# Kernel tuning notes

Hardware: AMD Instinct MI355X
Metric: run time of the kernel (lower is better)

Reference implementation:

```python
import jax, jax.numpy as jnp
import numpy as np

N_TAPERS = 3  # standard edgetaper iteration count used in vdeblur

def psf2otf(psf, shape):
    # zero-pad psf to `shape` and circularly shift so kernel center -> (0,0), then FFT
    kh, kw = psf.shape[-2], psf.shape[-1]
    pad = [(0, 0)] * (psf.ndim - 2) + [(0, shape[0] - kh), (0, shape[1] - kw)]
    p = jnp.pad(psf, pad)
    p = jnp.roll(p, shift=(-(kh // 2), -(kw // 2)), axis=(-2, -1))
    return jnp.fft.fft2(p)

def edgetaper_alpha(kernel, shape):
    # kernel: [kh,kw]; builds the separable taper window from kernel autocorrelation
    vs = []
    for i in range(2):
        proj = jnp.sum(kernel, axis=1 - i)
        z = jnp.fft.fft(proj, shape[i] - 1)
        z = jnp.fft.ifft(jnp.abs(z) ** 2).real
        z = jnp.concatenate([z, z[:1]])
        vs.append(1.0 - z / jnp.max(z))
    return jnp.outer(vs[0], vs[1])

def edgetaper_one(img, kernel):
    # img: [C,Hp,Wp], kernel: [kh,kw]; blend image with its circular blur near borders
    shape = img.shape[-2:]
    alpha = edgetaper_alpha(kernel, shape)[None]          # [1,Hp,Wp]
    otf = psf2otf(kernel, shape)[None]                    # [1,Hp,Wp] complex
    for _ in range(N_TAPERS):
        blurred = jnp.fft.ifft2(jnp.fft.fft2(img) * otf).real
        img = alpha * img + (1.0 - alpha) * blurred
    return img

def setup_inputs() -> dict:
    key = jax.random.key(0)
    k1, k2, k3, k4 = jax.random.split(key, 4)
    B, C, H, W = 8, 3, 512, 512
    KH = KW = 31
    NF, FS = 8, 3
    y = jax.random.uniform(k1, (B, C, H, W), dtype=jnp.float32)
    k = jax.random.uniform(k2, (B, 1, KH, KW), dtype=jnp.float32)
    k = k / jnp.sum(k, axis=(-2, -1), keepdims=True)       # normalized blur PSF
    lam = jax.random.uniform(k3, (), dtype=jnp.float32)    # nn.Parameter(torch.rand(1).squeeze())
    fan_in = C * FS * FS
    filters = jax.random.normal(k4, (NF, C, FS, FS), dtype=jnp.float32) * np.sqrt(2.0 / fan_in)
    return {"y": y, "k": k, "lam": lam, "filters": filters}

def reference(y, k, lam, filters):
    kh, kw = k.shape[-2], k.shape[-1]
    ph, pw = (kh - 1) // 2, (kw - 1) // 2
    # pad_for_kernel (edge replicate) + edgetaper
    x = jnp.pad(y, ((0, 0), (0, 0), (ph, ph), (pw, pw)), mode='edge')
    x = jax.vmap(edgetaper_one)(x, k[:, 0])
    H, W = x.shape[-2], x.shape[-1]
    Fy = jnp.fft.fft2(x)                                   # [B,C,H,W] complex (== rfft onesided=False)
    Dg = psf2otf(filters, (H, W))                          # [NF,C,H,W]
    Dk = psf2otf(k, (H, W))                                # [B,1,H,W], broadcasts over C
    exp_lam = jnp.exp(lam)
    Dg_sum = jnp.sum(jnp.abs(Dg) ** 2, axis=0)[None] * exp_lam   # [1,C,H,W]
    Omega = 1.0 / (jnp.abs(Dk) ** 2 + Dg_sum)              # [B,C,H,W]
    out = jnp.fft.ifft2(Omega * jnp.conj(Dk) * Fy).real    # irfft onesided=False
    return out
```

## Files before the change

### kernel.cpp

```cpp
#include <hip/hip_runtime.h>
#include <cmath>

#define HH 542
#define KH 271
#define NPIX (HH*HH)
#define RS 544
#define PPIX (HH*RS)
#define BB 8
#define CC3 3
#define NCH (BB*CC3)
#define NP 12
#define MROWS (NP*HH)
#define KSZ 31
#define KRAD 15
#define NF 8
#define FS 3

#define NSPLIT 2
#define NGRP 40
#define BTSZ (NGRP*NSPLIT*17*512)

typedef __attribute__((ext_vector_type(8))) short short8v;
typedef __attribute__((ext_vector_type(4))) float float4v;

static __device__ __forceinline__ float2 cmul(float2 a, float2 b) {
    return make_float2(a.x*b.x - a.y*b.y, a.x*b.y + a.y*b.x);
}

static __device__ __forceinline__ void pair_chans(int p, int& n1, int& n2) {
    if (p < 8) { n1 = 3*p;     n2 = 3*p + 1; }
    else       { int q = p-8; n1 = 6*q + 2; n2 = 6*q + 5; }
}

static __device__ __forceinline__ void split2_pack_pair(float x, float y,
        unsigned& p0, unsigned& p1) {
    unsigned ux = __float_as_uint(x), uy = __float_as_uint(y);
    unsigned hx0 = (ux + 0x8000u) & 0xffff0000u;
    unsigned hy0 = (uy + 0x8000u) & 0xffff0000u;
    float rx = x - __uint_as_float(hx0);
    float ry = y - __uint_as_float(hy0);
    unsigned hx1 = (__float_as_uint(rx) + 0x8000u) & 0xffff0000u;
    unsigned hy1 = (__float_as_uint(ry) + 0x8000u) & 0xffff0000u;
    p0 = (hx0 >> 16) | hy0;
    p1 = (hx1 >> 16) | hy1;
}

__global__ void gen_tables(float2* tw542, short* Btf, short* Bti) {
    int idx = blockIdx.x*blockDim.x + threadIdx.x;
    const float PI2 = 6.283185307179586f;
    if (idx < HH) {
        float ang = -PI2*(float)idx/(float)HH;
        float s, c; sincosf(ang, &s, &c);
        tw542[idx] = make_float2(c, s);
    }
    if (idx >= BTSZ) return;
    int j    = idx & 7;
    int lane = (idx >> 3) & 63;
    int rem  = idx >> 9;
    int step = rem % 17;
    int rem2 = rem / 17;
    int s    = rem2 % NSPLIT;
    int g    = rem2 / NSPLIT;
    if (g >= NGRP) return;
    int o  = (g >= 20) ? 1 : 0;
    int v1 = (g - 20*o)*16 + (lane & 15);
    int kq = step*32 + (lane >> 4)*8 + j;
    int kidx = kq >> 1, c = kq & 1;
    float wre = 0.f, wim = 0.f;
    if (v1 < KH && kidx < KH) {
        int r = (kidx*v1) % KH;
        float ang = -PI2*(float)r/(float)KH;
        float sn, cs; sincosf(ang, &sn, &cs);
        wre = cs; wim = sn;
    }
    float vf = (o==0) ? ((c==0) ? wre : -wim) : ((c==0) ?  wim : wre);
    float vi = (o==0) ? ((c==0) ? wre :  wim) : ((c==0) ? -wim : wre);
    {
        unsigned u = __float_as_uint(vf);
        unsigned h0 = (u + 0x8000u) & 0xffff0000u;
        float r1 = vf - __uint_as_float(h0);
        unsigned h1 = (__float_as_uint(r1) + 0x8000u) & 0xffff0000u;
        Btf[idx] = (short)(((s==0) ? h0 : h1) >> 16);
    }
    {
        unsigned u = __float_as_uint(vi);
        unsigned h0 = (u + 0x8000u) & 0xffff0000u;
        float r1 = vi - __uint_as_float(h0);
        unsigned h1 = (__float_as_uint(r1) + 0x8000u) & 0xffff0000u;
        Bti[idx] = (short)(((s==0) ? h0 : h1) >> 16);
    }
}

__global__ void alpha_kernel(const float* __restrict__ kk, float* __restrict__ valpha) {
    int b = blockIdx.x;
    int t = threadIdx.x;
    __shared__ float proj[2][KSZ];
    __shared__ float ac[2][KSZ];
    const float* kb = kk + b*KSZ*KSZ;
    if (t < KSZ) {
        float s = 0;
        for (int j = 0; j < KSZ; j++) s += kb[t*KSZ + j];
        proj[0][t] = s;
    } else if (t >= 32 && t < 32+KSZ) {
        int j = t - 32;
        float s = 0;
        for (int i = 0; i < KSZ; i++) s += kb[i*KSZ + j];
        proj[1][j] = s;
    }
    __syncthreads();
    if (t < KSZ) {
        float s0 = 0, s1 = 0;
        for (int m = 0; m + t < KSZ; m++) {
            s0 += proj[0][m]*proj[0][m+t];
            s1 += proj[1][m]*proj[1][m+t];
        }
        ac[0][t] = s0; ac[1][t] = s1;
    }
    __syncthreads();
    float inv0 = 1.0f/ac[0][0];
    float inv1 = 1.0f/ac[1][0];
    for (int d = t; d < HH; d += blockDim.x) {
        for (int a = 0; a < 2; a++) {
            float z;
            if (d <= 30)                   z = ac[a][d];
            else if (d >= 511 && d <= 540) z = ac[a][541-d];
            else if (d == 541)             z = ac[a][0];
            else                           z = 0.0f;
            valpha[(b*2 + a)*HH + d] = 1.0f - z*(a ? inv1 : inv0);
        }
    }
}

__global__ void dk_stage1(const float* __restrict__ kk, const float2* __restrict__ tw,
                          float2* __restrict__ T1) {
    int idx = blockIdx.x*blockDim.x + threadIdx.x;
    if (idx >= BB*KSZ*HH) return;
    int v  = idx % HH;
    int bm = idx / HH;
    int m  = bm % KSZ;
    int b  = bm / KSZ;
    const float* kb = kk + (b*KSZ + m)*KSZ;
    float2 w  = tw[(KRAD*(HH - v)) % HH];
    float2 ru = tw[v];
    float2 acc = make_float2(0.f, 0.f);
    for (int n = 0; n < KSZ; n++) {
        float kv = kb[n];
        acc.x = fmaf(kv, w.x, acc.x);
        acc.y = fmaf(kv, w.y, acc.y);
        float wx = w.x*ru.x - w.y*ru.y;
        float wy = w.x*ru.y + w.y*ru.x;
        w = make_float2(wx, wy);
    }
    T1[idx] = acc;
}

#define UT2 8
__global__ void dk_stage2(const float2* __restrict__ T1, const float2* __restrict__ tw,
                          float2* __restrict__ Dk) {
    int bid = blockIdx.x;
    int vc = bid % 3;
    int rem = bid / 3;
    int ut = rem % 68;
    int b  = rem / 68;
    int v = vc*256 + threadIdx.x;
    if (v >= HH) return;
    int u0 = ut*UT2;
    float2 acc[UT2], w[UT2], ru[UT2];
    #pragma unroll
    for (int uu = 0; uu < UT2; uu++) {
        int u = u0 + uu;
        int uc = (u < HH) ? u : 0;
        acc[uu] = make_float2(0.f, 0.f);
        w[uu]  = tw[(KRAD*(HH - uc)) % HH];
        ru[uu] = tw[uc];
    }
    const float2* t1 = T1 + (size_t)b*KSZ*HH + v;
    for (int m = 0; m < KSZ; m++) {
        float2 t = t1[(size_t)m*HH];
        #pragma unroll
        for (int uu = 0; uu < UT2; uu++) {
            acc[uu].x = fmaf(t.x, w[uu].x, fmaf(-t.y, w[uu].y, acc[uu].x));
            acc[uu].y = fmaf(t.x, w[uu].y, fmaf( t.y, w[uu].x, acc[uu].y));
            float wx = w[uu].x*ru[uu].x - w[uu].y*ru[uu].y;
            float wy = w[uu].x*ru[uu].y + w[uu].y*ru[uu].x;
            w[uu] = make_float2(wx, wy);
        }
    }
    #pragma unroll
    for (int uu = 0; uu < UT2; uu++) {
        int u = u0 + uu;
        if (u < HH) Dk[(size_t)b*NPIX + (size_t)u*HH + v] = acc[uu];
    }
}

__global__ void dgs_kernel(const float* __restrict__ filt, const float* __restrict__ lamp,
                           const float2* __restrict__ tw, float* __restrict__ Dgs) {
    int uv = blockIdx.x*blockDim.x + threadIdx.x;
    if (uv >= NPIX) return;
    int u = uv / HH;
    int v = uv - u*HH;
    float el = expf(lamp[0]);
    float2 wu[3], wv[3];
    wu[0] = tw[u ? HH-u : 0]; wu[1] = make_float2(1.f,0.f); wu[2] = tw[u];
    wv[0] = tw[v ? HH-v : 0]; wv[1] = make_float2(1.f,0.f); wv[2] = tw[v];
    float2 ph[3][3];
    #pragma unroll
    for (int m = 0; m < 3; m++)
        #pragma unroll
        for (int n = 0; n < 3; n++)
            ph[m][n] = cmul(wu[m], wv[n]);
    for (int c = 0; c < CC3; c++) {
        float s = 0.f;
        for (int f = 0; f < NF; f++) {
            float2 acc = make_float2(0.f, 0.f);
            const float* fp = filt + ((f*CC3 + c)*FS)*FS;
            #pragma unroll
            for (int m = 0; m < 3; m++)
                #pragma unroll
                for (int n = 0; n < 3; n++) {
                    float fv = fp[m*3+n];
                    acc.x = fmaf(fv, ph[m][n].x, acc.x);
                    acc.y = fmaf(fv, ph[m][n].y, acc.y);
                }
            s = fmaf(acc.x, acc.x, fmaf(acc.y, acc.y, s));
        }
        Dgs[c*NPIX + uv] = s*el;
    }
}

__global__ void pad_pack(const float* __restrict__ y, float* __restrict__ R0,
                         float2* __restrict__ CA) {
    int idx = blockIdx.x*blockDim.x + threadIdx.x;
    if (idx >= NP*NPIX) return;
    int uv = idx % NPIX;
    int p  = idx / NPIX;
    int n1, n2; pair_chans(p, n1, n2);
    int i = uv / HH, j = uv - i*HH;
    int yi = min(max(i - KRAD, 0), 511);
    int yj = min(max(j - KRAD, 0), 511);
    int yo = yi*512 + yj;
    float v1 = y[(size_t)n1*262144 + yo];
    float v2 = y[(size_t)n2*262144 + yo];
    size_t sp = (size_t)i*RS + j;
    R0[(size_t)n1*PPIX + sp] = v1;
    R0[(size_t)n2*PPIX + sp] = v2;
    CA[(size_t)p*PPIX + sp] = make_float2(v1, v2);
}

__global__ void specmul(const float2* __restrict__ CA, const float2* __restrict__ Dk,
                        const float* __restrict__ Dgs, float2* __restrict__ CB, int mode) {
    int idx = blockIdx.x*blockDim.x + threadIdx.x;
    if (idx >= NP*NPIX) return;
    int uv = idx % NPIX;
    int p  = idx / NPIX;
    int n1, n2; pair_chans(p, n1, n2);
    int b1 = n1/3, c1 = n1 - 3*b1;
    int b2 = n2/3, c2 = n2 - 3*b2;
    int i = uv / HH, j = uv - i*HH;
    int ni = i ? HH - i : 0;
    int nj = j ? HH - j : 0;
    float2 Z  = CA[(size_t)p*PPIX + (size_t)i*RS + j];
    float2 Zm = CA[(size_t)p*PPIX + (size_t)ni*RS + nj];
    float2 F1 = make_float2(0.5f*(Z.x + Zm.x), 0.5f*(Z.y - Zm.y));
    float2 F2 = make_float2(0.5f*(Z.y + Zm.y), 0.5f*(Zm.x - Z.x));
    float2 d1 = Dk[(size_t)b1*NPIX + uv];
    float2 d2 = Dk[(size_t)b2*NPIX + uv];
    float2 M1, M2;
    if (mode == 0) {
        M1 = d1; M2 = d2;
    } else {
        float o1 = 1.0f/(d1.x*d1.x + d1.y*d1.y + Dgs[(size_t)c1*NPIX + uv]);
        float o2 = 1.0f/(d2.x*d2.x + d2.y*d2.y + Dgs[(size_t)c2*NPIX + uv]);
        M1 = make_float2(d1.x*o1, -d1.y*o1);
        M2 = make_float2(d2.x*o2, -d2.y*o2);
    }
    float2 W1 = cmul(M1, F1);
    float2 W2 = cmul(M2, F2);
    CB[(size_t)p*PPIX + (size_t)i*RS + j] = make_float2(W1.x - W2.y, W1.y + W2.x);
}

__global__ void __launch_bounds__(256, 4)
fft_mfma(const float2* __restrict__ Ain, float2* __restrict__ Aout,
         const short* __restrict__ Bt, const float2* __restrict__ tw542,
         const float* __restrict__ valp, float* __restrict__ R0,
         float* __restrict__ outbuf, float scale, int conjtw, int mode)
{
    __shared__ char smem[17408];
    short* As = (short*)smem;
    float4* Tsf = (float4*)smem;
    const int APL = 64*40;

    int id = blockIdx.x;
    int xcd = id & 7, jj = id >> 3;
    int lin = xcd*128 + jj;
    if (lin >= 1020) return;
    int by = lin / 5, bx = lin - 5*by;

    int tid = threadIdx.x;
    int arow = tid >> 3, ai4 = tid & 7;
    int wid = tid >> 6, lane = tid & 63;
    int l15 = lane & 15, quad = lane >> 4;

    int aoff0 = l15*40 + quad*8;

    const short* pB[2];
    #pragma unroll
    for (int ct = 0; ct < 2; ct++) {
        int grp = (ct ? 20 : 0) + bx*4 + wid;
        pB[ct] = Bt + (size_t)grp*(NSPLIT*17*512) + lane*8;
    }

    float4v acc[4][2];
    #pragma unroll
    for (int mt = 0; mt < 4; mt++)
        #pragma unroll
        for (int ct = 0; ct < 2; ct++)
            acc[mt][ct] = (float4v)(0.f);

    float4 regA[2][2];
    short8v bf[2][2][2];
    const float4 z4 = make_float4(0.f,0.f,0.f,0.f);

    int rowg = by*32 + arow;
    bool rvld = rowg < MROWS;
    const float4* rp = (const float4*)Ain + (size_t)(rvld ? rowg : 0)*(RS/2);

    auto loadA = [&](int buf, int step) {
        int i0 = step*16 + 2*ai4;
        regA[buf][0] = (rvld && i0     < 271) ? rp[i0]   : z4;
        regA[buf][1] = (rvld && i0 + 1 < 271) ? rp[i0+1] : z4;
    };
    auto loadB = [&](int buf, int step) {
        #pragma unroll
        for (int ct = 0; ct < 2; ct++)
            #pragma unroll
            for (int s = 0; s < NSPLIT; s++)
                bf[buf][ct][s] = *(const short8v*)(pB[ct] + ((s*17 + step) << 9));
    };

    loadA(0, 0); loadB(0, 0);

    #pragma unroll 2
    for (int step = 0; step < 17; step++) {
        int cur = step & 1, nxt = cur ^ 1;
        {
            int rl = 2*arow;
            int offE = rl*40 + 4*ai4;
            float4 f0 = regA[cur][0], f1 = regA[cur][1];
            unsigned e0a,e1a, e0b,e1b;
            split2_pack_pair(f0.x, f0.y, e0a, e1a);
            split2_pack_pair(f1.x, f1.y, e0b, e1b);
            *(uint2*)(As + 0*APL + offE) = make_uint2(e0a, e0b);
            *(uint2*)(As + 1*APL + offE) = make_uint2(e1a, e1b);
            unsigned o0a,o1a, o0b,o1b;
            split2_pack_pair(f0.z, f0.w, o0a, o1a);
            split2_pack_pair(f1.z, f1.w, o0b, o1b);
            int offO = offE + 40;
            *(uint2*)(As + 0*APL + offO) = make_uint2(o0a, o0b);
            *(uint2*)(As + 1*APL + offO) = make_uint2(o1a, o1b);
        }
        __syncthreads();

        if (step + 1 < 17) { loadA(nxt, step+1); loadB(nxt, step+1); }

        #pragma unroll
        for (int sa = 0; sa < 2; sa++) {
            short8v af[4];
            #pragma unroll
            for (int mt = 0; mt < 4; mt++)
                af[mt] = *(const short8v*)(As + sa*APL + aoff0 + mt*16*40);
            #pragma unroll
            for (int sb = 0; sb + sa < 2; sb++)
                #pragma unroll
                for (int mt = 0; mt < 4; mt++)
                    #pragma unroll
                    for (int ct = 0; ct < 2; ct++)
                        acc[mt][ct] = __builtin_amdgcn_mfma_f32_16x16x32_bf16(
                            af[mt], bf[cur][ct][sb], acc[mt][ct], 0, 0, 0);
        }
        __syncthreads();
    }

    float2 tg;
    {
        int v1g = (bx*4 + wid)*16 + l15;
        tg = tw542[(v1g < HH) ? v1g : 0];
        if (conjtw) tg.y = -tg.y;
    }

    int lane16 = tid & 15;
    int rrow = tid >> 4;
    int r0 = by*32 + 2*lane16;
    bool rok = r0 < MROWS;
    int plane = rok ? (r0 / HH) : 0;
    int colg = r0 - plane*HH;
    int n1, n2; pair_chans(plane, n1, n2);
    int b1 = n1/3, b2 = n2/3;

    #pragma unroll
    for (int half = 0; half < 2; half++) {
        __syncthreads();
        #pragma unroll
        for (int mt = 0; mt < 4; mt++) {
            float2 v[2];
            #pragma unroll
            for (int pr = 0; pr < 2; pr++) {
                float Ere = acc[mt][0][2*pr], Ore = acc[mt][0][2*pr+1];
                float Eim = acc[mt][1][2*pr], Oim = acc[mt][1][2*pr+1];
                float tOre = tg.x*Ore - tg.y*Oim;
                float tOim = tg.x*Oim + tg.y*Ore;
                v[pr] = (half == 0)
                    ? make_float2((Ere + tOre)*scale, (Eim + tOim)*scale)
                    : make_float2((Ere - tOre)*scale, (Eim - tOim)*scale);
            }
            int v1loc = wid*16 + l15;
            int uu = mt*4 + quad;
            Tsf[v1loc*17 + uu] = make_float4(v[0].x, v[0].y, v[1].x, v[1].y);
        }
        __syncthreads();
        #pragma unroll
        for (int it = 0; it < 4; it++) {
            int v1loc = rrow + it*16;
            int v1g2 = bx*64 + v1loc;
            if (v1g2 >= KH || !rok) continue;
            int v1 = v1g2 + (half ? KH : 0);
            float4 f = Tsf[v1loc*17 + lane16];
            size_t sp = (size_t)v1*RS + colg;
            if (mode == 0) {
                *(float4*)(Aout + (size_t)plane*PPIX + sp) = f;
            } else if (mode == 1) {
                float ar1 = valp[b1*2*HH + v1];
                float ar2 = valp[b2*2*HH + v1];
                float ac1a = valp[(b1*2+1)*HH + colg];
                float ac1b = valp[(b1*2+1)*HH + colg + 1];
                float ac2a = valp[(b2*2+1)*HH + colg];
                float ac2b = valp[(b2*2+1)*HH + colg + 1];
                float2* p1 = (float2*)(R0 + (size_t)n1*PPIX + sp);
                float2* p2 = (float2*)(R0 + (size_t)n2*PPIX + sp);
                float2 o1 = *p1, o2 = *p2;
                float nv1a = fmaf(ar1*ac1a, o1.x - f.x, f.x);
                float nv1b = fmaf(ar1*ac1b, o1.y - f.z, f.z);
                float nv2a = fmaf(ar2*ac2a, o2.x - f.y, f.y);
                float nv2b = fmaf(ar2*ac2b, o2.y - f.w, f.w);
                *p1 = make_float2(nv1a, nv1b);
                *p2 = make_float2(nv2a, nv2b);
                *(float4*)(Aout + (size_t)plane*PPIX + sp) =
                    make_float4(nv1a, nv2a, nv1b, nv2b);
            } else {
                size_t so = (size_t)v1*HH + colg;
                *(float2*)(outbuf + (size_t)n1*NPIX + so) = make_float2(f.x, f.z);
                *(float2*)(outbuf + (size_t)n2*NPIX + so) = make_float2(f.y, f.w);
            }
        }
    }
}

extern "C" void kernel_launch(void* const* d_in, const int* in_sizes, int n_in,
                              void* d_out, int out_size, void* d_ws, size_t ws_size,
                              hipStream_t stream) {
    const float* y    = (const float*)d_in[0];
    const float* k    = (const float*)d_in[1];
    const float* lam  = (const float*)d_in[2];
    const float* filt = (const float*)d_in[3];
    float* out = (float*)d_out;

    char* base = (char*)d_ws;
    size_t off = 0;
    auto alloc = [&](size_t bytes) {
        void* p = base + off;
        off = (off + bytes + 511) & ~(size_t)511;
        return p;
    };
    float2* CA   = (float2*)alloc(sizeof(float2)*(size_t)NP*PPIX);
    float2* CB   = (float2*)alloc(sizeof(float2)*(size_t)NP*PPIX);
    float*  R0   = (float*) alloc(sizeof(float)*(size_t)NCH*PPIX);
    float2* Dk   = (float2*)alloc(sizeof(float2)*(size_t)BB*NPIX);
    float2* T1   = (float2*)alloc(sizeof(float2)*(size_t)BB*KSZ*HH);
    float*  Dgs  = (float*) alloc(sizeof(float)*(size_t)CC3*NPIX);
    short*  Btf  = (short*) alloc(sizeof(short)*(size_t)BTSZ);
    short*  Bti  = (short*) alloc(sizeof(short)*(size_t)BTSZ);
    float2* tw   = (float2*)alloc(sizeof(float2)*(size_t)HH);
    float*  valp = (float*) alloc(sizeof(float)*(size_t)BB*2*HH);
    (void)ws_size; (void)in_sizes; (void)n_in; (void)out_size;

    const int TPB = 256;
    auto nb = [](long n) { return (int)((n + 255)/256); };

    gen_tables<<<nb((long)BTSZ), TPB, 0, stream>>>(tw, Btf, Bti);
    alpha_kernel<<<BB, 64, 0, stream>>>(k, valp);
    dk_stage1<<<nb((long)BB*KSZ*HH), TPB, 0, stream>>>(k, tw, T1);
    dk_stage2<<<8*68*3, TPB, 0, stream>>>(T1, tw, Dk);
    dgs_kernel<<<nb((long)NPIX), TPB, 0, stream>>>(filt, lam, tw, Dgs);
    pad_pack<<<nb((long)NP*NPIX), TPB, 0, stream>>>(y, R0, CA);

    const int FG = 1024;
    const float isc = 1.0f/(float)HH;
    float2 *S = CA, *T = CB;
    fft_mfma<<<FG, TPB, 0, stream>>>(S, T, Btf, tw, valp, R0, out, 1.0f, 0, 0);
    fft_mfma<<<FG, TPB, 0, stream>>>(T, S, Btf, tw, valp, R0, out, 1.0f, 0, 0);
    for (int it = 0; it < 3; it++) {
        specmul<<<nb((long)NP*NPIX), TPB, 0, stream>>>(S, Dk, Dgs, T, 0);
        fft_mfma<<<FG, TPB, 0, stream>>>(T, S, Bti, tw, valp, R0, out, isc, 1, 0);
        fft_mfma<<<FG, TPB, 0, stream>>>(S, T, Bti, tw, valp, R0, out, isc, 1, 1);
        fft_mfma<<<FG, TPB, 0, stream>>>(T, S, Btf, tw, valp, R0, out, 1.0f, 0, 0);
        fft_mfma<<<FG, TPB, 0, stream>>>(S, T, Btf, tw, valp, R0, out, 1.0f, 0, 0);
        float2* tmp = S; S = T; T = tmp;
    }
    specmul<<<nb((long)NP*NPIX), TPB, 0, stream>>>(S, Dk, Dgs, T, 1);
    fft_mfma<<<FG, TPB, 0, stream>>>(T, S, Bti, tw, valp, R0, out, isc, 1, 0);
    fft_mfma<<<FG, TPB, 0, stream>>>(S, T, Bti, tw, valp, R0, out, isc, 1, 2);
}
```

Before: 749.3 us.

## Store intermediate FFT planes pre-split into bf16 hi/lo in MFMA-ready layout

Intermediate complex planes are now stored as pre-split bf16 hi/lo pairs, arranged so that fft_mfma can load A fragments straight from global memory into MFMA registers. This removes the LDS staging, the per-step split/pack work and the two __syncthreads per K step inside the GEMM loop. Producers (pad_pack, specmul, the fft epilogue) now do the split when they write, and specmul reconstructs floats when it reads. The buffers are zeroed with memsets so the padded rows and columns read as zero. In exchange, the A-operand loads lose the old software prefetch double-buffering and the global reads become more scattered.

```diff
diff --git a/kernel.cpp b/kernel.cpp
--- a/kernel.cpp
+++ b/kernel.cpp
@@ -16,6 +16,10 @@
 #define NF 8
 #define FS 3
 
+#define SROW 544
+#define SROWS_PL 13056
+#define SPL ((size_t)SROWS_PL*SROW)
+
 #define NSPLIT 2
 #define NGRP 40
 #define BTSZ (NGRP*NSPLIT*17*512)
@@ -43,6 +47,12 @@
     unsigned hy1 = (__float_as_uint(ry) + 0x8000u) & 0xffff0000u;
     p0 = (hx0 >> 16) | hy0;
     p1 = (hx1 >> 16) | hy1;
+}
+
+static __device__ __forceinline__ float2 unsplit_pair(unsigned h, unsigned l) {
+    float x = __uint_as_float(h << 16) + __uint_as_float(l << 16);
+    float y = __uint_as_float(h & 0xffff0000u) + __uint_as_float(l & 0xffff0000u);
+    return make_float2(x, y);
 }
 
 __global__ void gen_tables(float2* tw542, short* Btf, short* Bti) {
@@ -229,7 +239,7 @@
 }
 
 __global__ void pad_pack(const float* __restrict__ y, float* __restrict__ R0,
-                         float2* __restrict__ CA) {
+                         short* __restrict__ CAs) {
     int idx = blockIdx.x*blockDim.x + threadIdx.x;
     if (idx >= NP*NPIX) return;
     int uv = idx % NPIX;
@@ -241,14 +251,17 @@
     int yo = yi*512 + yj;
     float v1 = y[(size_t)n1*262144 + yo];
     float v2 = y[(size_t)n2*262144 + yo];
-    size_t sp = (size_t)i*RS + j;
-    R0[(size_t)n1*PPIX + sp] = v1;
-    R0[(size_t)n2*PPIX + sp] = v2;
-    CA[(size_t)p*PPIX + sp] = make_float2(v1, v2);
-}
-
-__global__ void specmul(const float2* __restrict__ CA, const float2* __restrict__ Dk,
-                        const float* __restrict__ Dgs, float2* __restrict__ CB, int mode) {
+    R0[(size_t)n1*PPIX + (size_t)i*RS + j] = v1;
+    R0[(size_t)n2*PPIX + (size_t)i*RS + j] = v2;
+    unsigned hi, lo; split2_pack_pair(v1, v2, hi, lo);
+    size_t row = 2*((size_t)p*HH + i) + (size_t)(j & 1);
+    size_t col = (size_t)(j & ~1);
+    *(unsigned*)(CAs + row*SROW + col)       = hi;
+    *(unsigned*)(CAs + SPL + row*SROW + col) = lo;
+}
+
+__global__ void specmul(const short* __restrict__ CAs, const float2* __restrict__ Dk,
+                        const float* __restrict__ Dgs, short* __restrict__ CBs, int mode) {
     int idx = blockIdx.x*blockDim.x + threadIdx.x;
     if (idx >= NP*NPIX) return;
     int uv = idx % NPIX;
@@ -259,8 +272,16 @@
     int i = uv / HH, j = uv - i*HH;
     int ni = i ? HH - i : 0;
     int nj = j ? HH - j : 0;
-    float2 Z  = CA[(size_t)p*PPIX + (size_t)i*RS + j];
-    float2 Zm = CA[(size_t)p*PPIX + (size_t)ni*RS + nj];
+    size_t rz = 2*((size_t)p*HH + i) + (size_t)(j & 1);
+    size_t cz = (size_t)(j & ~1);
+    size_t rm = 2*((size_t)p*HH + ni) + (size_t)(nj & 1);
+    size_t cm = (size_t)(nj & ~1);
+    unsigned zh = *(const unsigned*)(CAs + rz*SROW + cz);
+    unsigned zl = *(const unsigned*)(CAs + SPL + rz*SROW + cz);
+    unsigned mh = *(const unsigned*)(CAs + rm*SROW + cm);
+    unsigned ml = *(const unsigned*)(CAs + SPL + rm*SROW + cm);
+    float2 Z  = unsplit_pair(zh, zl);
+    float2 Zm = unsplit_pair(mh, ml);
     float2 F1 = make_float2(0.5f*(Z.x + Zm.x), 0.5f*(Z.y - Zm.y));
     float2 F2 = make_float2(0.5f*(Z.y + Zm.y), 0.5f*(Zm.x - Z.x));
     float2 d1 = Dk[(size_t)b1*NPIX + uv];
@@ -276,19 +297,19 @@
     }
     float2 W1 = cmul(M1, F1);
     float2 W2 = cmul(M2, F2);
-    CB[(size_t)p*PPIX + (size_t)i*RS + j] = make_float2(W1.x - W2.y, W1.y + W2.x);
+    float2 out = make_float2(W1.x - W2.y, W1.y + W2.x);
+    unsigned hi, lo; split2_pack_pair(out.x, out.y, hi, lo);
+    *(unsigned*)(CBs + rz*SROW + cz)       = hi;
+    *(unsigned*)(CBs + SPL + rz*SROW + cz) = lo;
 }
 
 __global__ void __launch_bounds__(256, 4)
-fft_mfma(const float2* __restrict__ Ain, float2* __restrict__ Aout,
+fft_mfma(const short* __restrict__ Ains, short* __restrict__ Aouts,
          const short* __restrict__ Bt, const float2* __restrict__ tw542,
          const float* __restrict__ valp, float* __restrict__ R0,
          float* __restrict__ outbuf, float scale, int conjtw, int mode)
 {
-    __shared__ char smem[17408];
-    short* As = (short*)smem;
-    float4* Tsf = (float4*)smem;
-    const int APL = 64*40;
+    __shared__ float4 Tsf[64*17];
 
     int id = blockIdx.x;
     int xcd = id & 7, jj = id >> 3;
@@ -297,11 +318,17 @@
     int by = lin / 5, bx = lin - 5*by;
 
     int tid = threadIdx.x;
-    int arow = tid >> 3, ai4 = tid & 7;
     int wid = tid >> 6, lane = tid & 63;
     int l15 = lane & 15, quad = lane >> 4;
 
-    int aoff0 = l15*40 + quad*8;
+    const short* pA[2][4];
+    #pragma unroll
+    for (int sa = 0; sa < 2; sa++)
+        #pragma unroll
+        for (int mt = 0; mt < 4; mt++) {
+            size_t rl = (size_t)by*64 + (size_t)(l15 + mt*16);
+            pA[sa][mt] = Ains + (size_t)sa*SPL + rl*SROW + quad*8;
+        }
 
     const short* pB[2];
     #pragma unroll
@@ -317,58 +344,21 @@
         for (int ct = 0; ct < 2; ct++)
             acc[mt][ct] = (float4v)(0.f);
 
-    float4 regA[2][2];
-    short8v bf[2][2][2];
-    const float4 z4 = make_float4(0.f,0.f,0.f,0.f);
-
-    int rowg = by*32 + arow;
-    bool rvld = rowg < MROWS;
-    const float4* rp = (const float4*)Ain + (size_t)(rvld ? rowg : 0)*(RS/2);
-
-    auto loadA = [&](int buf, int step) {
-        int i0 = step*16 + 2*ai4;
-        regA[buf][0] = (rvld && i0     < 271) ? rp[i0]   : z4;
-        regA[buf][1] = (rvld && i0 + 1 < 271) ? rp[i0+1] : z4;
-    };
-    auto loadB = [&](int buf, int step) {
+    #pragma unroll 2
+    for (int step = 0; step < 17; step++) {
+        short8v af[2][4], bfv[2][2];
+        #pragma unroll
+        for (int sa = 0; sa < 2; sa++)
+            #pragma unroll
+            for (int mt = 0; mt < 4; mt++)
+                af[sa][mt] = *(const short8v*)(pA[sa][mt] + step*32);
         #pragma unroll
         for (int ct = 0; ct < 2; ct++)
             #pragma unroll
             for (int s = 0; s < NSPLIT; s++)
-                bf[buf][ct][s] = *(const short8v*)(pB[ct] + ((s*17 + step) << 9));
-    };
-
-    loadA(0, 0); loadB(0, 0);
-
-    #pragma unroll 2
-    for (int step = 0; step < 17; step++) {
-        int cur = step & 1, nxt = cur ^ 1;
-        {
-            int rl = 2*arow;
-            int offE = rl*40 + 4*ai4;
-            float4 f0 = regA[cur][0], f1 = regA[cur][1];
-            unsigned e0a,e1a, e0b,e1b;
-            split2_pack_pair(f0.x, f0.y, e0a, e1a);
-            split2_pack_pair(f1.x, f1.y, e0b, e1b);
-            *(uint2*)(As + 0*APL + offE) = make_uint2(e0a, e0b);
-            *(uint2*)(As + 1*APL + offE) = make_uint2(e1a, e1b);
-            unsigned o0a,o1a, o0b,o1b;
-            split2_pack_pair(f0.z, f0.w, o0a, o1a);
-            split2_pack_pair(f1.z, f1.w, o0b, o1b);
-            int offO = offE + 40;
-            *(uint2*)(As + 0*APL + offO) = make_uint2(o0a, o0b);
-            *(uint2*)(As + 1*APL + offO) = make_uint2(o1a, o1b);
-        }
-        __syncthreads();
-
-        if (step + 1 < 17) { loadA(nxt, step+1); loadB(nxt, step+1); }
-
-        #pragma unroll
-        for (int sa = 0; sa < 2; sa++) {
-            short8v af[4];
-            #pragma unroll
-            for (int mt = 0; mt < 4; mt++)
-                af[mt] = *(const short8v*)(As + sa*APL + aoff0 + mt*16*40);
+                bfv[ct][s] = *(const short8v*)(pB[ct] + ((s*17 + step) << 9));
+        #pragma unroll
+        for (int sa = 0; sa < 2; sa++)
             #pragma unroll
             for (int sb = 0; sb + sa < 2; sb++)
                 #pragma unroll
@@ -376,9 +366,7 @@
                     #pragma unroll
                     for (int ct = 0; ct < 2; ct++)
                         acc[mt][ct] = __builtin_amdgcn_mfma_f32_16x16x32_bf16(
-                            af[mt], bf[cur][ct][sb], acc[mt][ct], 0, 0, 0);
-        }
-        __syncthreads();
+                            af[sa][mt], bfv[ct][sb], acc[mt][ct], 0, 0, 0);
     }
 
     float2 tg;
@@ -425,9 +413,16 @@
             if (v1g2 >= KH || !rok) continue;
             int v1 = v1g2 + (half ? KH : 0);
             float4 f = Tsf[v1loc*17 + lane16];
-            size_t sp = (size_t)v1*RS + colg;
+            size_t Rout = (size_t)plane*HH + v1;
+            size_t re = 2*Rout;
             if (mode == 0) {
-                *(float4*)(Aout + (size_t)plane*PPIX + sp) = f;
+                unsigned h0,l0,h1,l1;
+                split2_pack_pair(f.x, f.y, h0, l0);
+                split2_pack_pair(f.z, f.w, h1, l1);
+                *(unsigned*)(Aouts + re*SROW + colg)             = h0;
+                *(unsigned*)(Aouts + (re+1)*SROW + colg)         = h1;
+                *(unsigned*)(Aouts + SPL + re*SROW + colg)       = l0;
+                *(unsigned*)(Aouts + SPL + (re+1)*SROW + colg)   = l1;
             } else if (mode == 1) {
                 float ar1 = valp[b1*2*HH + v1];
                 float ar2 = valp[b2*2*HH + v1];
@@ -435,6 +430,7 @@
                 float ac1b = valp[(b1*2+1)*HH + colg + 1];
                 float ac2a = valp[(b2*2+1)*HH + colg];
                 float ac2b = valp[(b2*2+1)*HH + colg + 1];
+                size_t sp = (size_t)v1*RS + colg;
                 float2* p1 = (float2*)(R0 + (size_t)n1*PPIX + sp);
                 float2* p2 = (float2*)(R0 + (size_t)n2*PPIX + sp);
                 float2 o1 = *p1, o2 = *p2;
@@ -444,8 +440,13 @@
                 float nv2b = fmaf(ar2*ac2b, o2.y - f.w, f.w);
                 *p1 = make_float2(nv1a, nv1b);
                 *p2 = make_float2(nv2a, nv2b);
-                *(float4*)(Aout + (size_t)plane*PPIX + sp) =
-                    make_float4(nv1a, nv2a, nv1b, nv2b);
+                unsigned h0,l0,h1,l1;
+                split2_pack_pair(nv1a, nv2a, h0, l0);
+                split2_pack_pair(nv1b, nv2b, h1, l1);
+                *(unsigned*)(Aouts + re*SROW + colg)             = h0;
+                *(unsigned*)(Aouts + (re+1)*SROW + colg)         = h1;
+                *(unsigned*)(Aouts + SPL + re*SROW + colg)       = l0;
+                *(unsigned*)(Aouts + SPL + (re+1)*SROW + colg)   = l1;
             } else {
                 size_t so = (size_t)v1*HH + colg;
                 *(float2*)(outbuf + (size_t)n1*NPIX + so) = make_float2(f.x, f.z);
@@ -471,8 +472,8 @@
         off = (off + bytes + 511) & ~(size_t)511;
         return p;
     };
-    float2* CA   = (float2*)alloc(sizeof(float2)*(size_t)NP*PPIX);
-    float2* CB   = (float2*)alloc(sizeof(float2)*(size_t)NP*PPIX);
+    short*  CAs  = (short*) alloc(sizeof(short)*2*SPL);
+    short*  CBs  = (short*) alloc(sizeof(short)*2*SPL);
     float*  R0   = (float*) alloc(sizeof(float)*(size_t)NCH*PPIX);
     float2* Dk   = (float2*)alloc(sizeof(float2)*(size_t)BB*NPIX);
     float2* T1   = (float2*)alloc(sizeof(float2)*(size_t)BB*KSZ*HH);
@@ -486,16 +487,19 @@
     const int TPB = 256;
     auto nb = [](long n) { return (int)((n + 255)/256); };
 
+    hipMemsetAsync(CAs, 0, sizeof(short)*2*SPL, stream);
+    hipMemsetAsync(CBs, 0, sizeof(short)*2*SPL, stream);
+
     gen_tables<<<nb((long)BTSZ), TPB, 0, stream>>>(tw, Btf, Bti);
     alpha_kernel<<<BB, 64, 0, stream>>>(k, valp);
     dk_stage1<<<nb((long)BB*KSZ*HH), TPB, 0, stream>>>(k, tw, T1);
     dk_stage2<<<8*68*3, TPB, 0, stream>>>(T1, tw, Dk);
     dgs_kernel<<<nb((long)NPIX), TPB, 0, stream>>>(filt, lam, tw, Dgs);
-    pad_pack<<<nb((long)NP*NPIX), TPB, 0, stream>>>(y, R0, CA);
+    pad_pack<<<nb((long)NP*NPIX), TPB, 0, stream>>>(y, R0, CAs);
 
     const int FG = 1024;
     const float isc = 1.0f/(float)HH;
-    float2 *S = CA, *T = CB;
+    short *S = CAs, *T = CBs;
     fft_mfma<<<FG, TPB, 0, stream>>>(S, T, Btf, tw, valp, R0, out, 1.0f, 0, 0);
     fft_mfma<<<FG, TPB, 0, stream>>>(T, S, Btf, tw, valp, R0, out, 1.0f, 0, 0);
     for (int it = 0; it < 3; it++) {
@@ -504,7 +508,7 @@
         fft_mfma<<<FG, TPB, 0, stream>>>(S, T, Bti, tw, valp, R0, out, isc, 1, 1);
         fft_mfma<<<FG, TPB, 0, stream>>>(T, S, Btf, tw, valp, R0, out, 1.0f, 0, 0);
         fft_mfma<<<FG, TPB, 0, stream>>>(S, T, Btf, tw, valp, R0, out, 1.0f, 0, 0);
-        float2* tmp = S; S = T; T = tmp;
+        short* tmp = S; S = T; T = tmp;
     }
     specmul<<<nb((long)NP*NPIX), TPB, 0, stream>>>(S, Dk, Dgs, T, 1);
     fft_mfma<<<FG, TPB, 0, stream>>>(T, S, Bti, tw, valp, R0, out, isc, 1, 0);
```

New measurement: 1.075 ms. +43.4%, slower.
